# Kernel tuning notes

Hardware: AMD Instinct MI355X
Metric: run time of the kernel (lower is better)

## Reference

```python
import jax, jax.numpy as jnp
import numpy as np

B, S, V, D = 8, 1024, 8192, 256
MAX_POS = 1024


def _positional_encoding(position, d_model):
    pos = np.arange(position)[:, None].astype(np.float32)
    i = np.arange(d_model)[None, :].astype(np.float32)
    angle_rads = pos / np.power(10000.0, 2.0 * np.floor(i / 2.0) / np.float32(d_model))
    angle_rads[:, 0::2] = np.sin(angle_rads[:, 0::2])
    angle_rads[:, 1::2] = np.cos(angle_rads[:, 1::2])
    return jnp.asarray(angle_rads[None, ...], dtype=jnp.float32)  # [1, position, d_model]


def setup_inputs() -> dict:
    key = jax.random.key(0)
    k1, k2 = jax.random.split(key)
    x = jax.random.randint(k1, (B, S, V), 0, 2, dtype=jnp.int32)  # multi-hot mask
    emb_table = jax.random.normal(k2, (V, D), dtype=jnp.float32) * 0.02
    pos_enc = _positional_encoding(MAX_POS, D)
    return {"x": x, "emb_table": emb_table, "pos_enc": pos_enc}


def reference(x, emb_table, pos_enc):
    # Multi-hot embedding-bag: sum_v x[b,s,v] * emb_table[v,:]  (dense O(V) reduction,
    # faithful to get_emb's full-vocab embed * mask + reduce_sum)
    seq_len = x.shape[1]
    d_model = emb_table.shape[1]
    xf = x.astype(jnp.float32)
    emb = jnp.einsum('bsv,vd->bsd', xf, emb_table)
    emb = emb * jnp.sqrt(jnp.float32(d_model))
    # positional encoding gated by whether the position has any active token
    any_tok = (jnp.sum(x, axis=-1) > 0).astype(jnp.float32)[..., None]  # [B,S,1]
    out = emb + pos_enc[:, :seq_len, :] * any_tok
    # dropout is identity in eval mode; num_layers = 0 -> no encoder layers
    return out
```

## Files before the change

### kernel.cpp

```cpp
#include <hip/hip_runtime.h>
#include <stdint.h>


#define K_TOT 8192
#define D_DIM 256
#define KSPLIT 8
#define KCHUNK (K_TOT / KSPLIT)
#define BK 64
#define TROWS 128
#define NTILES (KCHUNK / BK)
#define PART_STRIDE (8192u * 256u)

typedef short  short8  __attribute__((ext_vector_type(8)));
typedef float  floatx4 __attribute__((ext_vector_type(4)));
typedef int    intx4   __attribute__((ext_vector_type(4)));

union S8U { intx4 i; short8 s; };

#define WS_PART_OFF (4u * 1024u * 1024u)
#define WS_RS_OFF   (68u * 1024u * 1024u)

__device__ __forceinline__ unsigned int bf16_rne(float f) {
    unsigned int u = __float_as_uint(f);
    u += 0x7fffu + ((u >> 16) & 1u);
    return u >> 16;
}

__device__ __forceinline__ void load_lds16(const int* g, int* l) {
    __builtin_amdgcn_global_load_lds((const __attribute__((address_space(1))) unsigned int*)g,
                                     (__attribute__((address_space(3))) unsigned int*)l,
                                     16, 0, 0);
}

__global__ __launch_bounds__(256) void prep_kernel(const float* __restrict__ emb,
                                                   unsigned short* __restrict__ wsBf) {
    int gid = blockIdx.x * 256 + threadIdx.x;
    int l  = gid & 63;
    int kb = (gid >> 6) & 255;
    int c  = gid >> 14;
    int d  = c * 16 + (l & 15);
    int v0 = kb * 32 + (l >> 4) * 8;
    const float* src = emb + (size_t)v0 * D_DIM + d;
    intx4 q;
#pragma unroll
    for (int p = 0; p < 4; ++p) {
        unsigned int u0 = bf16_rne(src[(size_t)(2 * p) * D_DIM] * 16.0f);
        unsigned int u1 = bf16_rne(src[(size_t)(2 * p + 1) * D_DIM] * 16.0f);
        q[p] = (int)(u0 | (u1 << 16));
    }
    *(intx4*)(wsBf + (size_t)gid * 8) = q;
}

__global__ __launch_bounds__(512, 4) void gemm_kernel(const int* __restrict__ x,
                                                      const unsigned short* __restrict__ wsBf,
                                                      float* __restrict__ part,
                                                      int* __restrict__ rsp) {
    __shared__ int Al[2][TROWS * 64];

    const int m0   = blockIdx.x * TROWS;
    const int kidx = blockIdx.y;
    const int kbeg = kidx * KCHUNK;
    const int t    = threadIdx.x;
    const int wave = t >> 6, lane = t & 63;
    const int wr   = wave >> 2, wc = wave & 3;
    const int quad = lane >> 4, rl = lane & 15;
    const int sx   = rl & 7;

    const int srow = t >> 4;
    const int sg   = (t & 15) ^ (srow & 7);
    const int* gA  = x + (size_t)(m0 + srow) * K_TOT + kbeg + sg * 4;
    int* const ldst = &Al[0][srow * 64 + (t & 15) * 4];

    floatx4 acc[4][4];
#pragma unroll
    for (int i = 0; i < 4; ++i)
#pragma unroll
        for (int j = 0; j < 4; ++j) acc[i][j] = (floatx4){0.f, 0.f, 0.f, 0.f};
    int rp[4] = {0, 0, 0, 0};

    const int kbase = kidx * (KCHUNK / 32);

#pragma unroll
    for (int r = 0; r < 4; ++r)
        load_lds16(gA + (size_t)(r * 32) * K_TOT, ldst + r * 32 * 64);

    for (int tl = 0; tl < NTILES; ++tl) {
        __syncthreads();
        if (tl + 1 < NTILES) {
            const int* g = gA + (tl + 1) * BK;
            int* dst = ldst + ((tl + 1) & 1) * (TROWS * 64);
#pragma unroll
            for (int r = 0; r < 4; ++r)
                load_lds16(g + (size_t)(r * 32) * K_TOT, dst + r * 32 * 64);
        }
        const int* buf = &Al[tl & 1][0];

#pragma unroll
        for (int s = 0; s < 2; ++s) {
            const int kb = kbase + tl * 2 + s;

            short8 bf[4];
#pragma unroll
            for (int j = 0; j < 4; ++j)
                bf[j] = ((const S8U*)(wsBf + ((size_t)((wc * 4 + j) * 256 + kb) * 64 + lane) * 8))->s;

            short8 af[4];
#pragma unroll
            for (int i = 0; i < 4; ++i) {
                const int row = wr * 64 + i * 16 + rl;
                const int g0  = s * 8 + quad * 2;
                intx4 v0 = *(const intx4*)(buf + row * 64 + ((g0 ^ sx) * 4));
                intx4 v1 = *(const intx4*)(buf + row * 64 + (((g0 + 1) ^ sx) * 4));
                int p0 = v0[0] | (v0[1] << 16);
                int p1 = v0[2] | (v0[3] << 16);
                int p2 = v1[0] | (v1[1] << 16);
                int p3 = v1[2] | (v1[3] << 16);
                if (wc == 0) rp[i] += p0 + p1 + p2 + p3;
                S8U u;
                u.i[0] = p0 * 0x3F80;
                u.i[1] = p1 * 0x3F80;
                u.i[2] = p2 * 0x3F80;
                u.i[3] = p3 * 0x3F80;
                af[i] = u.s;
            }

#pragma unroll
            for (int i = 0; i < 4; ++i)
#pragma unroll
                for (int j = 0; j < 4; ++j)
                    acc[i][j] = __builtin_amdgcn_mfma_f32_16x16x32_bf16(af[i], bf[j], acc[i][j], 0, 0, 0);
        }
    }

    if (wc == 0) {
#pragma unroll
        for (int i = 0; i < 4; ++i) {
            int cnt = (rp[i] & 0xFFFF) + ((unsigned)rp[i] >> 16);
            cnt += __shfl_xor(cnt, 16);
            cnt += __shfl_xor(cnt, 32);
            if (quad == 0) rsp[(size_t)kidx * 8192 + m0 + wr * 64 + i * 16 + rl] = cnt;
        }
    }

    float* pk = part + (size_t)kidx * PART_STRIDE;
#pragma unroll
    for (int i = 0; i < 4; ++i) {
#pragma unroll
        for (int j = 0; j < 4; ++j) {
            int col = wc * 64 + j * 16 + rl;
#pragma unroll
            for (int r = 0; r < 4; ++r) {
                int row = m0 + wr * 64 + i * 16 + quad * 4 + r;
                pk[(size_t)row * D_DIM + col] = acc[i][j][r];
            }
        }
    }
}

__global__ __launch_bounds__(256) void reduce_kernel(const float* __restrict__ part,
                                                     const int* __restrict__ rsp,
                                                     const float* __restrict__ pos,
                                                     float* __restrict__ out) {
    int gid = blockIdx.x * 256 + threadIdx.x;
    size_t base = (size_t)gid * 4;
    int row = gid >> 6;
    floatx4 a = *(const floatx4*)(part + base);
    int rsum = rsp[row];
#pragma unroll
    for (int k = 1; k < KSPLIT; ++k) {
        a += *(const floatx4*)(part + (size_t)k * PART_STRIDE + base);
        rsum += rsp[(size_t)k * 8192 + row];
    }
    if (rsum > 0) {
        int s = row & 1023;
        int col = (gid & 63) * 4;
        a += *(const floatx4*)(pos + (size_t)s * D_DIM + col);
    }
    *(floatx4*)(out + base) = a;
}

extern "C" void kernel_launch(void* const* d_in, const int* in_sizes, int n_in,
                              void* d_out, int out_size, void* d_ws, size_t ws_size,
                              hipStream_t stream) {
    const int*   x   = (const int*)d_in[0];
    const float* emb = (const float*)d_in[1];
    const float* pos = (const float*)d_in[2];
    float*       out = (float*)d_out;

    unsigned short* wsBf = (unsigned short*)d_ws;
    float*          part = (float*)((char*)d_ws + WS_PART_OFF);
    int*            rsp  = (int*)((char*)d_ws + WS_RS_OFF);

    prep_kernel<<<dim3(1024), dim3(256), 0, stream>>>(emb, wsBf);
    gemm_kernel<<<dim3(64, KSPLIT), dim3(512), 0, stream>>>(x, wsBf, part, rsp);
    reduce_kernel<<<dim3(2048), dim3(256), 0, stream>>>(part, rsp, pos, out);
}
```

Before: 461.2 us.

## Stage B tiles in LDS, shrink M tile, stagger K phase per block

Reorders the prepared bf16 weight layout so each 32-wide K slice is contiguous, then stages both the x tile and the weight tile in LDS with double-buffered async global-to-LDS loads instead of reading weights directly from global memory per wave. The tile shrinks to 64 rows with 256 threads and 1024 blocks, and each block starts its K loop at a staggered phase to spread accesses across memory channels. The goal is better weight reuse and coalescing and fewer simultaneous hits on the same addresses. In exchange each tile carries half as much K per barrier, so there are more synchronisations, and the x tile is smaller, so weight traffic per output row rises.

```diff
diff --git a/kernel.cpp b/kernel.cpp
--- a/kernel.cpp
+++ b/kernel.cpp
@@ -5,10 +5,9 @@
 #define K_TOT 8192
 #define D_DIM 256
 #define KSPLIT 8
-#define KCHUNK (K_TOT / KSPLIT)
-#define BK 64
-#define TROWS 128
-#define NTILES (KCHUNK / BK)
+#define KCHUNK 1024
+#define BK 32
+#define NT 32
 #define PART_STRIDE (8192u * 256u)
 
 typedef short  short8  __attribute__((ext_vector_type(8)));
@@ -33,11 +32,11 @@
 }
 
 __global__ __launch_bounds__(256) void prep_kernel(const float* __restrict__ emb,
-                                                   unsigned short* __restrict__ wsBf) {
+                                                   unsigned short* __restrict__ wsBt) {
     int gid = blockIdx.x * 256 + threadIdx.x;
     int l  = gid & 63;
-    int kb = (gid >> 6) & 255;
-    int c  = gid >> 14;
+    int c  = (gid >> 6) & 15;
+    int kb = gid >> 10;
     int d  = c * 16 + (l & 15);
     int v0 = kb * 32 + (l >> 4) * 8;
     const float* src = emb + (size_t)v0 * D_DIM + d;
@@ -48,28 +47,29 @@
         unsigned int u1 = bf16_rne(src[(size_t)(2 * p + 1) * D_DIM] * 16.0f);
         q[p] = (int)(u0 | (u1 << 16));
     }
-    *(intx4*)(wsBf + (size_t)gid * 8) = q;
-}
-
-__global__ __launch_bounds__(512, 4) void gemm_kernel(const int* __restrict__ x,
-                                                      const unsigned short* __restrict__ wsBf,
-                                                      float* __restrict__ part,
-                                                      int* __restrict__ rsp) {
-    __shared__ int Al[2][TROWS * 64];
-
-    const int m0   = blockIdx.x * TROWS;
-    const int kidx = blockIdx.y;
+    *(intx4*)(wsBt + (size_t)gid * 8) = q;
+}
+
+__global__ __launch_bounds__(256) void gemm_kernel(const int* __restrict__ x,
+                                                   const unsigned short* __restrict__ wsBt,
+                                                   float* __restrict__ part,
+                                                   int* __restrict__ rsp) {
+    __shared__ int   Al[2][2048];
+    __shared__ short Bl[2][8192];
+
+    const int mb = blockIdx.x, kidx = blockIdx.y;
+    const int m0 = mb * 64;
     const int kbeg = kidx * KCHUNK;
-    const int t    = threadIdx.x;
+    const int phase = (mb * 7 + kidx * 9) & (NT - 1);
+    const int t = threadIdx.x;
     const int wave = t >> 6, lane = t & 63;
-    const int wr   = wave >> 2, wc = wave & 3;
     const int quad = lane >> 4, rl = lane & 15;
-    const int sx   = rl & 7;
-
-    const int srow = t >> 4;
-    const int sg   = (t & 15) ^ (srow & 7);
-    const int* gA  = x + (size_t)(m0 + srow) * K_TOT + kbeg + sg * 4;
-    int* const ldst = &Al[0][srow * 64 + (t & 15) * 4];
+
+    const int arow = t >> 3, aslot = t & 7;
+    const int asg  = aslot ^ (arow & 7);
+    const int* gA = x + (size_t)(m0 + arow) * K_TOT + kbeg + asg * 4;
+
+    const int kbase = kidx * NT;
 
     floatx4 acc[4][4];
 #pragma unroll
@@ -78,67 +78,70 @@
         for (int j = 0; j < 4; ++j) acc[i][j] = (floatx4){0.f, 0.f, 0.f, 0.f};
     int rp[4] = {0, 0, 0, 0};
 
-    const int kbase = kidx * (KCHUNK / 32);
-
-#pragma unroll
-    for (int r = 0; r < 4; ++r)
-        load_lds16(gA + (size_t)(r * 32) * K_TOT, ldst + r * 32 * 64);
-
-    for (int tl = 0; tl < NTILES; ++tl) {
+    {
+        const int p0 = phase;
+        load_lds16(gA + p0 * BK, &Al[0][t * 4]);
+        load_lds16(gA + (size_t)32 * K_TOT + p0 * BK, &Al[0][1024 + t * 4]);
+        const unsigned short* bs = wsBt + (size_t)(kbase + p0) * 8192;
+#pragma unroll
+        for (int r = 0; r < 4; ++r)
+            load_lds16((const int*)(bs + (r * 256 + t) * 8), (int*)&Bl[0][(r * 256 + t) * 8]);
+    }
+
+    for (int tl = 0; tl < NT; ++tl) {
+        const int pcur = (tl + phase) & (NT - 1);
         __syncthreads();
-        if (tl + 1 < NTILES) {
-            const int* g = gA + (tl + 1) * BK;
-            int* dst = ldst + ((tl + 1) & 1) * (TROWS * 64);
+        if (tl + 1 < NT) {
+            const int pn = (tl + 1 + phase) & (NT - 1);
+            const int b = (tl + 1) & 1;
+            load_lds16(gA + pn * BK, &Al[b][t * 4]);
+            load_lds16(gA + (size_t)32 * K_TOT + pn * BK, &Al[b][1024 + t * 4]);
+            const unsigned short* bs = wsBt + (size_t)(kbase + pn) * 8192;
 #pragma unroll
             for (int r = 0; r < 4; ++r)
-                load_lds16(g + (size_t)(r * 32) * K_TOT, dst + r * 32 * 64);
-        }
-        const int* buf = &Al[tl & 1][0];
-
-#pragma unroll
-        for (int s = 0; s < 2; ++s) {
-            const int kb = kbase + tl * 2 + s;
-
-            short8 bf[4];
+                load_lds16((const int*)(bs + (r * 256 + t) * 8), (int*)&Bl[b][(r * 256 + t) * 8]);
+        }
+        const int cur = tl & 1;
+
+        short8 bf[4];
+#pragma unroll
+        for (int j = 0; j < 4; ++j)
+            bf[j] = *(const short8*)&Bl[cur][((wave * 4 + j) * 64 + lane) * 8];
+
+        short8 af[4];
+#pragma unroll
+        for (int i = 0; i < 4; ++i) {
+            const int row = i * 16 + rl;
+            const int* base = &Al[cur][row * 32];
+            intx4 v0 = *(const intx4*)(base + (((quad * 2)     ^ (row & 7)) * 4));
+            intx4 v1 = *(const intx4*)(base + (((quad * 2 + 1) ^ (row & 7)) * 4));
+            int p0 = v0[0] | (v0[1] << 16);
+            int p1 = v0[2] | (v0[3] << 16);
+            int p2 = v1[0] | (v1[1] << 16);
+            int p3 = v1[2] | (v1[3] << 16);
+            if (wave == 0) rp[i] += p0 + p1 + p2 + p3;
+            S8U u;
+            u.i[0] = p0 * 0x3F80;
+            u.i[1] = p1 * 0x3F80;
+            u.i[2] = p2 * 0x3F80;
+            u.i[3] = p3 * 0x3F80;
+            af[i] = u.s;
+        }
+
+#pragma unroll
+        for (int i = 0; i < 4; ++i)
 #pragma unroll
             for (int j = 0; j < 4; ++j)
-                bf[j] = ((const S8U*)(wsBf + ((size_t)((wc * 4 + j) * 256 + kb) * 64 + lane) * 8))->s;
-
-            short8 af[4];
-#pragma unroll
-            for (int i = 0; i < 4; ++i) {
-                const int row = wr * 64 + i * 16 + rl;
-                const int g0  = s * 8 + quad * 2;
-                intx4 v0 = *(const intx4*)(buf + row * 64 + ((g0 ^ sx) * 4));
-                intx4 v1 = *(const intx4*)(buf + row * 64 + (((g0 + 1) ^ sx) * 4));
-                int p0 = v0[0] | (v0[1] << 16);
-                int p1 = v0[2] | (v0[3] << 16);
-                int p2 = v1[0] | (v1[1] << 16);
-                int p3 = v1[2] | (v1[3] << 16);
-                if (wc == 0) rp[i] += p0 + p1 + p2 + p3;
-                S8U u;
-                u.i[0] = p0 * 0x3F80;
-                u.i[1] = p1 * 0x3F80;
-                u.i[2] = p2 * 0x3F80;
-                u.i[3] = p3 * 0x3F80;
-                af[i] = u.s;
-            }
-
-#pragma unroll
-            for (int i = 0; i < 4; ++i)
-#pragma unroll
-                for (int j = 0; j < 4; ++j)
-                    acc[i][j] = __builtin_amdgcn_mfma_f32_16x16x32_bf16(af[i], bf[j], acc[i][j], 0, 0, 0);
-        }
-    }
-
-    if (wc == 0) {
+                acc[i][j] = __builtin_amdgcn_mfma_f32_16x16x32_bf16(af[i], bf[j], acc[i][j], 0, 0, 0);
+    }
+
+    if (wave == 0) {
 #pragma unroll
         for (int i = 0; i < 4; ++i) {
             int cnt = (rp[i] & 0xFFFF) + ((unsigned)rp[i] >> 16);
             cnt += __shfl_xor(cnt, 16);
             cnt += __shfl_xor(cnt, 32);
-            if (quad == 0) rsp[(size_t)kidx * 8192 + m0 + wr * 64 + i * 16 + rl] = cnt;
+            if (quad == 0) rsp[(size_t)kidx * 8192 + m0 + i * 16 + rl] = cnt;
         }
     }
 
@@ -147,10 +150,10 @@
     for (int i = 0; i < 4; ++i) {
 #pragma unroll
         for (int j = 0; j < 4; ++j) {
-            int col = wc * 64 + j * 16 + rl;
+            int col = wave * 64 + j * 16 + rl;
 #pragma unroll
             for (int r = 0; r < 4; ++r) {
-                int row = m0 + wr * 64 + i * 16 + quad * 4 + r;
+                int row = m0 + i * 16 + quad * 4 + r;
                 pk[(size_t)row * D_DIM + col] = acc[i][j][r];
             }
         }
@@ -187,11 +190,11 @@
     const float* pos = (const float*)d_in[2];
     float*       out = (float*)d_out;
 
-    unsigned short* wsBf = (unsigned short*)d_ws;
+    unsigned short* wsBt = (unsigned short*)d_ws;
     float*          part = (float*)((char*)d_ws + WS_PART_OFF);
     int*            rsp  = (int*)((char*)d_ws + WS_RS_OFF);
 
-    prep_kernel<<<dim3(1024), dim3(256), 0, stream>>>(emb, wsBf);
-    gemm_kernel<<<dim3(64, KSPLIT), dim3(512), 0, stream>>>(x, wsBf, part, rsp);
+    prep_kernel<<<dim3(1024), dim3(256), 0, stream>>>(emb, wsBt);
+    gemm_kernel<<<dim3(128, KSPLIT), dim3(256), 0, stream>>>(x, wsBt, part, rsp);
     reduce_kernel<<<dim3(2048), dim3(256), 0, stream>>>(part, rsp, pos, out);
 }
```

After: 426.7 us. -7.5%, faster.
